# Kernel optimization log

Hardware: AMD Instinct MI355X
Metric: run time of the kernel (lower is better)

## Reference

```python
import jax, jax.numpy as jnp
import numpy as np

SEQ_LEN = 16384
IN_DIM = 2048
STATE_DIM = 2048


def setup_inputs() -> dict:
    key = jax.random.key(0)
    k_xs, k_lam, k_win, k_c, k_d = jax.random.split(key, 5)
    xs = jax.random.normal(k_xs, (SEQ_LEN, IN_DIM), dtype=jnp.float32)
    # diagonal state-transition values in (0, 1) for stability
    lam = jax.random.uniform(k_lam, (STATE_DIM,), dtype=jnp.float32)
    w_in = jax.random.normal(k_win, (STATE_DIM, IN_DIM), dtype=jnp.float32) / np.float32(np.sqrt(IN_DIM))
    c_out = jax.random.normal(k_c, (IN_DIM, STATE_DIM), dtype=jnp.float32) / np.float32(np.sqrt(STATE_DIM))
    d_skip = jax.random.normal(k_d, (IN_DIM,), dtype=jnp.float32)
    return {"xs": xs, "lam": lam, "w_in": w_in, "c_out": c_out, "d_skip": d_skip}


def _ssm_cell(a, b):
    # Faithful replication of BaseSSMLayer.ssm_cell (including its use of
    # matrix_pow_i * matrix_pow_i for the first component, exactly as in source).
    matrix_pow_i, bx_i = a
    matrix_pow_j, bx_j = b
    return (matrix_pow_i * matrix_pow_i, matrix_pow_j * bx_i + bx_j)


def reference(xs, lam, w_in, c_out, d_skip):
    seq_len = xs.shape[0]
    # discretize: broadcast diagonal lambda over the sequence -> [L, N]
    lambda_elements = jnp.broadcast_to(lam, (seq_len, lam.shape[0]))
    # preprocess_inputs: vmap(w_in @ x) == xs @ w_in.T  -> [L, N]
    w_in_xs = jnp.einsum('li,ni->ln', xs, w_in)
    _, hs = jax.lax.associative_scan(_ssm_cell, (lambda_elements, w_in_xs))
    # postprocess: y_t = C h_t + D * x_t  -> [L, in_dim]
    return jnp.einsum('ln,on->lo', hs, c_out) + xs * d_skip
```

## Files before the change

kernel.cpp:

```cpp
#include <hip/hip_runtime.h>
#include <hip/hip_bf16.h>

#define SEQ   16384
#define DIM   2048
#define CHUNK 256
#define NCHUNK (SEQ / CHUNK)

typedef __attribute__((ext_vector_type(8))) short  short8;
typedef __attribute__((ext_vector_type(4))) short  short4v;
typedef __attribute__((ext_vector_type(4))) float  floatx4;

static __device__ __forceinline__ float bf2f(short s) {
    return __uint_as_float(((unsigned)(unsigned short)s) << 16);
}
static __device__ __forceinline__ short f2bf(float f) {
    unsigned u = __float_as_uint(f);
    u += 0x7fff + ((u >> 16) & 1);
    return (short)(u >> 16);
}

__global__ void cast_kernel(const float* __restrict__ in, short* __restrict__ out, int n4) {
    int i = blockIdx.x * blockDim.x + threadIdx.x;
    if (i >= n4) return;
    float4 v = ((const float4*)in)[i];
    short4v s;
    s.x = f2bf(v.x); s.y = f2bf(v.y); s.z = f2bf(v.z); s.w = f2bf(v.w);
    ((short4v*)out)[i] = s;
}

template<int FUSE>
__global__ __launch_bounds__(256, 2)
void gemm_bt(const short* __restrict__ A, const short* __restrict__ B,
             short* __restrict__ Cbf, float* __restrict__ Cf,
             const float* __restrict__ xs, const float* __restrict__ dskip)
{
    constexpr int K = DIM;
    __shared__ alignas(16) short As[128 * 32];
    __shared__ alignas(16) short Bs[128 * 32];

    const int tid = threadIdx.x;
    const int m0  = blockIdx.y * 128;
    const int n0  = blockIdx.x * 128;

    const int c0 = tid, c1 = tid + 256;
    const short* ga0 = A + (size_t)(m0 + (c0 >> 2)) * K + (c0 & 3) * 8;
    const short* ga1 = A + (size_t)(m0 + (c1 >> 2)) * K + (c1 & 3) * 8;
    const short* gb0 = B + (size_t)(n0 + (c0 >> 2)) * K + (c0 & 3) * 8;
    const short* gb1 = B + (size_t)(n0 + (c1 >> 2)) * K + (c1 & 3) * 8;
    short* la0 = &As[c0 * 8];
    short* la1 = &As[c1 * 8];
    short* lb0 = &Bs[c0 * 8];
    short* lb1 = &Bs[c1 * 8];

    const int lane = tid & 63;
    const int wv   = tid >> 6;
    const int wm   = (wv >> 1) * 64;
    const int wn   = (wv & 1) * 64;
    const int l16  = lane & 15;
    const int quad = lane >> 4;

    floatx4 acc[4][4] = {};

    for (int kk = 0; kk < K; kk += 32) {
        __builtin_amdgcn_global_load_lds(ga0 + kk, la0, 16, 0, 0);
        __builtin_amdgcn_global_load_lds(ga1 + kk, la1, 16, 0, 0);
        __builtin_amdgcn_global_load_lds(gb0 + kk, lb0, 16, 0, 0);
        __builtin_amdgcn_global_load_lds(gb1 + kk, lb1, 16, 0, 0);
        __syncthreads();

        short8 aV[4], bV[4];
        #pragma unroll
        for (int i = 0; i < 4; i++)
            aV[i] = *(const short8*)&As[(wm + i * 16 + l16) * 32 + quad * 8];
        #pragma unroll
        for (int i = 0; i < 4; i++)
            bV[i] = *(const short8*)&Bs[(wn + i * 16 + l16) * 32 + quad * 8];

        #pragma unroll
        for (int mi = 0; mi < 4; mi++)
            #pragma unroll
            for (int ni = 0; ni < 4; ni++)
                acc[mi][ni] = __builtin_amdgcn_mfma_f32_16x16x32_bf16(
                    aV[mi], bV[ni], acc[mi][ni], 0, 0, 0);
        __syncthreads();
    }

    if (FUSE == 0) {
        #pragma unroll
        for (int mi = 0; mi < 4; mi++) {
            int rb = m0 + wm + mi * 16 + quad * 4;
            #pragma unroll
            for (int ni = 0; ni < 4; ni++) {
                int cc = n0 + wn + ni * 16 + l16;
                #pragma unroll
                for (int r = 0; r < 4; r++)
                    Cbf[(size_t)(rb + r) * DIM + cc] = f2bf(acc[mi][ni][r]);
            }
        }
    } else {
        float dsk[4];
        #pragma unroll
        for (int ni = 0; ni < 4; ni++) dsk[ni] = dskip[n0 + wn + ni * 16 + l16];
        #pragma unroll
        for (int mi = 0; mi < 4; mi++) {
            int rb = m0 + wm + mi * 16 + quad * 4;
            #pragma unroll
            for (int ni = 0; ni < 4; ni++) {
                int cc = n0 + wn + ni * 16 + l16;
                #pragma unroll
                for (int r = 0; r < 4; r++) {
                    size_t idx = (size_t)(rb + r) * DIM + cc;
                    Cf[idx] = acc[mi][ni][r] + xs[idx] * dsk[ni];
                }
            }
        }
    }
}

__global__ void scan_pass1(const short* __restrict__ bx, const float* __restrict__ lam,
                           float* __restrict__ blockLast)
{
    int n     = blockIdx.x * 256 + threadIdx.x;
    int chunk = blockIdx.y;
    float lm  = lam[n];
    const short* p = bx + (size_t)chunk * CHUNK * DIM + n;
    float h = 0.f;
    #pragma unroll 8
    for (int i = 0; i < CHUNK; i++)
        h = fmaf(lm, h, bf2f(p[(size_t)i * DIM]));
    blockLast[(size_t)chunk * DIM + n] = h;
}

__global__ void scan_pass2(float* __restrict__ blockLast, const float* __restrict__ lam)
{
    int n    = blockIdx.x * 256 + threadIdx.x;
    float lm = lam[n];
    float p  = lm;
    #pragma unroll
    for (int i = 0; i < 8; i++) p = p * p;
    float carry = 0.f;
    for (int c = 0; c < NCHUNK; c++) {
        float t = blockLast[(size_t)c * DIM + n];
        blockLast[(size_t)c * DIM + n] = carry;
        carry = fmaf(p, carry, t);
    }
}

__global__ void scan_pass3(short* __restrict__ bxh, const float* __restrict__ lam,
                           const float* __restrict__ carry)
{
    int n     = blockIdx.x * 256 + threadIdx.x;
    int chunk = blockIdx.y;
    float lm  = lam[n];
    float h   = carry[(size_t)chunk * DIM + n];
    short* p  = bxh + (size_t)chunk * CHUNK * DIM + n;
    #pragma unroll 8
    for (int i = 0; i < CHUNK; i++) {
        h = fmaf(lm, h, bf2f(p[(size_t)i * DIM]));
        p[(size_t)i * DIM] = f2bf(h);
    }
}

extern "C" void kernel_launch(void* const* d_in, const int* in_sizes, int n_in,
                              void* d_out, int out_size, void* d_ws, size_t ws_size,
                              hipStream_t stream)
{
    const float* xs    = (const float*)d_in[0];
    const float* lam   = (const float*)d_in[1];
    const float* w_in  = (const float*)d_in[2];
    const float* c_out = (const float*)d_in[3];
    const float* dskip = (const float*)d_in[4];
    float* out = (float*)d_out;

    char*  ws    = (char*)d_ws;
    short* bxh   = (short*)ws;
    short* w_bf  = (short*)(ws + (size_t)64 * 1024 * 1024);
    short* c_bf  = (short*)(ws + (size_t)72 * 1024 * 1024);
    float* blkl  = (float*)(ws + (size_t)80 * 1024 * 1024);
    short* xs_bf = (short*)d_out;

    cast_kernel<<<SEQ * DIM / 4 / 256, 256, 0, stream>>>(xs, xs_bf, SEQ * DIM / 4);
    cast_kernel<<<DIM * DIM / 4 / 256, 256, 0, stream>>>(w_in, w_bf, DIM * DIM / 4);
    cast_kernel<<<DIM * DIM / 4 / 256, 256, 0, stream>>>(c_out, c_bf, DIM * DIM / 4);

    dim3 ggrid(DIM / 128, SEQ / 128);
    gemm_bt<0><<<ggrid, 256, 0, stream>>>(xs_bf, w_bf, bxh, nullptr, nullptr, nullptr);

    dim3 sgrid(DIM / 256, NCHUNK);
    scan_pass1<<<sgrid, 256, 0, stream>>>(bxh, lam, blkl);
    scan_pass2<<<DIM / 256, 256, 0, stream>>>(blkl, lam);
    scan_pass3<<<sgrid, 256, 0, stream>>>(bxh, lam, blkl);

    gemm_bt<1><<<ggrid, 256, 0, stream>>>(bxh, c_bf, nullptr, out, xs, dskip);
}
```

Baseline: 629.1 us.

## Rewrite GEMM as 256x256 double-buffered swizzled pipeline and vectorize scan

Replaces the 128x128, 256-thread GEMM with a 256x256 tile, 512-thread kernel. It uses BK=64, double-buffered LDS with XOR swizzling, interleaved async global-to-LDS staging, and MFMA phases with raised wave priority and explicit waitcnt/barriers. The scan kernels now process two state channels per thread with 32-bit loads and stores, the chunk size is halved, and the carry buffer moves into unused output memory. This aims to raise MFMA utilization and cut LDS and global load overhead, at the cost of large LDS use (128KB per block), complex fragile synchronisation, and reliance on spare output space.

New measurement: 571.2 us. 9.2% less time.

```diff
diff --git a/kernel.cpp b/kernel.cpp
--- a/kernel.cpp
+++ b/kernel.cpp
@@ -1,9 +1,8 @@
 #include <hip/hip_runtime.h>
-#include <hip/hip_bf16.h>
 
 #define SEQ   16384
 #define DIM   2048
-#define CHUNK 256
+#define CHUNK 128
 #define NCHUNK (SEQ / CHUNK)
 
 typedef __attribute__((ext_vector_type(8))) short  short8;
@@ -28,89 +27,174 @@
     ((short4v*)out)[i] = s;
 }
 
+
+#define BAR   __builtin_amdgcn_s_barrier()
+#define PRIO1 __builtin_amdgcn_s_setprio(1)
+#define PRIO0 __builtin_amdgcn_s_setprio(0)
+#define LGKM0 do { asm volatile("s_waitcnt lgkmcnt(0)" ::: "memory"); \
+                   __builtin_amdgcn_sched_barrier(0); } while (0)
+#define VMC6  asm volatile("s_waitcnt vmcnt(6)" ::: "memory")
+#define VMC0  asm volatile("s_waitcnt vmcnt(0)" ::: "memory")
+
+#define STAGE_A(b, h, t) do { \
+    const short* _s = Abase + (size_t)(h) * 128 * K + (size_t)(t) * 64; \
+    __builtin_amdgcn_global_load_lds(_s + gOff0, &As[b][h][c0 * 8], 16, 0, 0); \
+    __builtin_amdgcn_global_load_lds(_s + gOff1, &As[b][h][c1 * 8], 16, 0, 0); \
+} while (0)
+#define STAGE_B(b, h, t) do { \
+    const short* _s = Bbase + (size_t)(h) * 128 * K + (size_t)(t) * 64; \
+    __builtin_amdgcn_global_load_lds(_s + gOff0, &Bs[b][h][c0 * 8], 16, 0, 0); \
+    __builtin_amdgcn_global_load_lds(_s + gOff1, &Bs[b][h][c1 * 8], 16, 0, 0); \
+} while (0)
+
+#define LDA(b, mh) \
+    _Pragma("unroll") \
+    for (int mi = 0; mi < 4; mi++) { \
+        _Pragma("unroll") \
+        for (int ks = 0; ks < 2; ks++) \
+            aV[mi][ks] = *(const short8*)&As[b][mh][(arow + mi * 16) * 64 + \
+                                                    ((((ks << 2) | quad) ^ sx) << 3)]; \
+    }
+#define LDB(dst, b, nh) \
+    _Pragma("unroll") \
+    for (int ni = 0; ni < 2; ni++) { \
+        _Pragma("unroll") \
+        for (int ks = 0; ks < 2; ks++) \
+            dst[ni][ks] = *(const short8*)&Bs[b][nh][(brow + ni * 16) * 64 + \
+                                                     ((((ks << 2) | quad) ^ sx) << 3)]; \
+    }
+#define MMA(mh, nh, bR) \
+    _Pragma("unroll") \
+    for (int mi = 0; mi < 4; mi++) { \
+        _Pragma("unroll") \
+        for (int ni = 0; ni < 2; ni++) { \
+            acc[mh][nh][mi][ni] = __builtin_amdgcn_mfma_f32_16x16x32_bf16( \
+                aV[mi][0], bR[ni][0], acc[mh][nh][mi][ni], 0, 0, 0); \
+            acc[mh][nh][mi][ni] = __builtin_amdgcn_mfma_f32_16x16x32_bf16( \
+                aV[mi][1], bR[ni][1], acc[mh][nh][mi][ni], 0, 0, 0); \
+        } \
+    }
+
 template<int FUSE>
-__global__ __launch_bounds__(256, 2)
+__global__ __launch_bounds__(512, 2)
 void gemm_bt(const short* __restrict__ A, const short* __restrict__ B,
              short* __restrict__ Cbf, float* __restrict__ Cf,
              const float* __restrict__ xs, const float* __restrict__ dskip)
 {
-    constexpr int K = DIM;
-    __shared__ alignas(16) short As[128 * 32];
-    __shared__ alignas(16) short Bs[128 * 32];
+    constexpr int K  = DIM;
+    constexpr int NT = K / 64;
+
+    __shared__ alignas(16) short As[2][2][128 * 64];
+    __shared__ alignas(16) short Bs[2][2][128 * 64];
 
     const int tid = threadIdx.x;
-    const int m0  = blockIdx.y * 128;
-    const int n0  = blockIdx.x * 128;
-
-    const int c0 = tid, c1 = tid + 256;
-    const short* ga0 = A + (size_t)(m0 + (c0 >> 2)) * K + (c0 & 3) * 8;
-    const short* ga1 = A + (size_t)(m0 + (c1 >> 2)) * K + (c1 & 3) * 8;
-    const short* gb0 = B + (size_t)(n0 + (c0 >> 2)) * K + (c0 & 3) * 8;
-    const short* gb1 = B + (size_t)(n0 + (c1 >> 2)) * K + (c1 & 3) * 8;
-    short* la0 = &As[c0 * 8];
-    short* la1 = &As[c1 * 8];
-    short* lb0 = &Bs[c0 * 8];
-    short* lb1 = &Bs[c1 * 8];
+    const int m0  = blockIdx.y * 256;
+    const int n0  = blockIdx.x * 256;
 
     const int lane = tid & 63;
     const int wv   = tid >> 6;
-    const int wm   = (wv >> 1) * 64;
-    const int wn   = (wv & 1) * 64;
+    const int wrow = wv >> 2;
+    const int wcol = wv & 3;
     const int l16  = lane & 15;
     const int quad = lane >> 4;
-
-    floatx4 acc[4][4] = {};
-
-    for (int kk = 0; kk < K; kk += 32) {
-        __builtin_amdgcn_global_load_lds(ga0 + kk, la0, 16, 0, 0);
-        __builtin_amdgcn_global_load_lds(ga1 + kk, la1, 16, 0, 0);
-        __builtin_amdgcn_global_load_lds(gb0 + kk, lb0, 16, 0, 0);
-        __builtin_amdgcn_global_load_lds(gb1 + kk, lb1, 16, 0, 0);
-        __syncthreads();
-
-        short8 aV[4], bV[4];
-        #pragma unroll
-        for (int i = 0; i < 4; i++)
-            aV[i] = *(const short8*)&As[(wm + i * 16 + l16) * 32 + quad * 8];
-        #pragma unroll
-        for (int i = 0; i < 4; i++)
-            bV[i] = *(const short8*)&Bs[(wn + i * 16 + l16) * 32 + quad * 8];
-
-        #pragma unroll
-        for (int mi = 0; mi < 4; mi++)
-            #pragma unroll
-            for (int ni = 0; ni < 4; ni++)
-                acc[mi][ni] = __builtin_amdgcn_mfma_f32_16x16x32_bf16(
-                    aV[mi], bV[ni], acc[mi][ni], 0, 0, 0);
-        __syncthreads();
-    }
+    const int sx   = l16 & 7;
+    const int arow = wrow * 64 + l16;
+    const int brow = wcol * 32 + l16;
+
+    const int c0 = tid, c1 = tid + 512;
+    const int r0 = c0 >> 3, r1 = c1 >> 3;
+    const size_t gOff0 = (size_t)r0 * K + (size_t)((((c0 & 7) ^ (r0 & 7))) * 8);
+    const size_t gOff1 = (size_t)r1 * K + (size_t)((((c1 & 7) ^ (r1 & 7))) * 8);
+    const short* Abase = A + (size_t)m0 * K;
+    const short* Bbase = B + (size_t)n0 * K;
+
+    short8  aV[4][2], bA[2][2], bB[2][2];
+    floatx4 acc[2][2][4][2] = {};
+
+    STAGE_A(0, 0, 0); STAGE_B(0, 0, 0); STAGE_B(0, 1, 0); STAGE_A(0, 1, 0);
+    STAGE_A(1, 0, 1); STAGE_B(1, 0, 1); STAGE_B(1, 1, 1);
+    VMC6;
+    BAR;
+
+    for (int i = 0; i < NT / 2; ++i) {
+        const int t1 = 2 * i + 1;
+        const int t2 = (2 * i + 2) & (NT - 1);
+        const int t3 = (2 * i + 3) & (NT - 1);
+
+        LDA(0, 0); LDB(bA, 0, 0); STAGE_A(1, 1, t1);
+        BAR; LGKM0;
+        PRIO1; MMA(0, 0, bA); PRIO0;
+        BAR;
+        LDB(bB, 0, 1); STAGE_A(0, 0, t2);
+        BAR; LGKM0;
+        PRIO1; MMA(0, 1, bB); PRIO0;
+        BAR;
+        LDA(0, 1); STAGE_B(0, 0, t2);
+        BAR; LGKM0;
+        PRIO1; MMA(1, 0, bA); PRIO0;
+        BAR;
+        STAGE_B(0, 1, t2);
+        BAR;
+        PRIO1; MMA(1, 1, bB); PRIO0;
+        VMC6;
+        BAR;
+        LDA(1, 0); LDB(bA, 1, 0); STAGE_A(0, 1, t2);
+        BAR; LGKM0;
+        PRIO1; MMA(0, 0, bA); PRIO0;
+        BAR;
+        LDB(bB, 1, 1); STAGE_A(1, 0, t3);
+        BAR; LGKM0;
+        PRIO1; MMA(0, 1, bB); PRIO0;
+        BAR;
+        LDA(1, 1); STAGE_B(1, 0, t3);
+        BAR; LGKM0;
+        PRIO1; MMA(1, 0, bA); PRIO0;
+        BAR;
+        STAGE_B(1, 1, t3);
+        BAR;
+        PRIO1; MMA(1, 1, bB); PRIO0;
+        VMC6;
+        BAR;
+    }
+    VMC0;
 
     if (FUSE == 0) {
         #pragma unroll
+        for (int mh = 0; mh < 2; mh++)
+        #pragma unroll
         for (int mi = 0; mi < 4; mi++) {
-            int rb = m0 + wm + mi * 16 + quad * 4;
-            #pragma unroll
-            for (int ni = 0; ni < 4; ni++) {
-                int cc = n0 + wn + ni * 16 + l16;
+            const int rb = m0 + wrow * 64 + mh * 128 + mi * 16 + quad * 4;
+            #pragma unroll
+            for (int nh = 0; nh < 2; nh++)
+            #pragma unroll
+            for (int ni = 0; ni < 2; ni++) {
+                const int cc = n0 + wcol * 32 + nh * 128 + ni * 16 + l16;
                 #pragma unroll
                 for (int r = 0; r < 4; r++)
-                    Cbf[(size_t)(rb + r) * DIM + cc] = f2bf(acc[mi][ni][r]);
+                    Cbf[(size_t)(rb + r) * DIM + cc] = f2bf(acc[mh][nh][mi][ni][r]);
             }
         }
     } else {
-        float dsk[4];
-        #pragma unroll
-        for (int ni = 0; ni < 4; ni++) dsk[ni] = dskip[n0 + wn + ni * 16 + l16];
+        float dsk[2][2];
+        #pragma unroll
+        for (int nh = 0; nh < 2; nh++)
+        #pragma unroll
+        for (int ni = 0; ni < 2; ni++)
+            dsk[nh][ni] = dskip[n0 + wcol * 32 + nh * 128 + ni * 16 + l16];
+        #pragma unroll
+        for (int mh = 0; mh < 2; mh++)
         #pragma unroll
         for (int mi = 0; mi < 4; mi++) {
-            int rb = m0 + wm + mi * 16 + quad * 4;
-            #pragma unroll
-            for (int ni = 0; ni < 4; ni++) {
-                int cc = n0 + wn + ni * 16 + l16;
+            const int rb = m0 + wrow * 64 + mh * 128 + mi * 16 + quad * 4;
+            #pragma unroll
+            for (int nh = 0; nh < 2; nh++)
+            #pragma unroll
+            for (int ni = 0; ni < 2; ni++) {
+                const int cc = n0 + wcol * 32 + nh * 128 + ni * 16 + l16;
                 #pragma unroll
                 for (int r = 0; r < 4; r++) {
                     size_t idx = (size_t)(rb + r) * DIM + cc;
-                    Cf[idx] = acc[mi][ni][r] + xs[idx] * dsk[ni];
+                    Cf[idx] = acc[mh][nh][mi][ni][r] + xs[idx] * dsk[nh][ni];
                 }
             }
         }
@@ -120,44 +204,58 @@
 __global__ void scan_pass1(const short* __restrict__ bx, const float* __restrict__ lam,
                            float* __restrict__ blockLast)
 {
-    int n     = blockIdx.x * 256 + threadIdx.x;
+    int n2    = blockIdx.x * 256 + threadIdx.x;
+    int n     = n2 * 2;
     int chunk = blockIdx.y;
-    float lm  = lam[n];
-    const short* p = bx + (size_t)chunk * CHUNK * DIM + n;
-    float h = 0.f;
-    #pragma unroll 8
-    for (int i = 0; i < CHUNK; i++)
-        h = fmaf(lm, h, bf2f(p[(size_t)i * DIM]));
-    blockLast[(size_t)chunk * DIM + n] = h;
+    float lm0 = lam[n], lm1 = lam[n + 1];
+    const unsigned* p = (const unsigned*)(bx + (size_t)chunk * CHUNK * DIM) + n2;
+    float h0 = 0.f, h1 = 0.f;
+    #pragma unroll 16
+    for (int i = 0; i < CHUNK; i++) {
+        unsigned v = p[(size_t)i * (DIM / 2)];
+        h0 = fmaf(lm0, h0, bf2f((short)(v & 0xffffu)));
+        h1 = fmaf(lm1, h1, bf2f((short)(v >> 16)));
+    }
+    float2 o; o.x = h0; o.y = h1;
+    *(float2*)&blockLast[(size_t)chunk * DIM + n] = o;
 }
 
 __global__ void scan_pass2(float* __restrict__ blockLast, const float* __restrict__ lam)
 {
-    int n    = blockIdx.x * 256 + threadIdx.x;
-    float lm = lam[n];
-    float p  = lm;
+    int n2 = blockIdx.x * 256 + threadIdx.x;
+    int n  = n2 * 2;
+    float lm0 = lam[n], lm1 = lam[n + 1];
+    float p0 = lm0, p1 = lm1;
     #pragma unroll
-    for (int i = 0; i < 8; i++) p = p * p;
-    float carry = 0.f;
+    for (int i = 0; i < 7; i++) { p0 *= p0; p1 *= p1; }
+    float c0 = 0.f, c1 = 0.f;
     for (int c = 0; c < NCHUNK; c++) {
-        float t = blockLast[(size_t)c * DIM + n];
-        blockLast[(size_t)c * DIM + n] = carry;
-        carry = fmaf(p, carry, t);
+        float2* q = (float2*)&blockLast[(size_t)c * DIM + n];
+        float2 t = *q;
+        float2 w; w.x = c0; w.y = c1;
+        *q = w;
+        c0 = fmaf(p0, c0, t.x);
+        c1 = fmaf(p1, c1, t.y);
     }
 }
 
 __global__ void scan_pass3(short* __restrict__ bxh, const float* __restrict__ lam,
                            const float* __restrict__ carry)
 {
-    int n     = blockIdx.x * 256 + threadIdx.x;
+    int n2    = blockIdx.x * 256 + threadIdx.x;
+    int n     = n2 * 2;
     int chunk = blockIdx.y;
-    float lm  = lam[n];
-    float h   = carry[(size_t)chunk * DIM + n];
-    short* p  = bxh + (size_t)chunk * CHUNK * DIM + n;
-    #pragma unroll 8
+    float lm0 = lam[n], lm1 = lam[n + 1];
+    float h0  = carry[(size_t)chunk * DIM + n];
+    float h1  = carry[(size_t)chunk * DIM + n + 1];
+    unsigned* p = (unsigned*)(bxh + (size_t)chunk * CHUNK * DIM) + n2;
+    #pragma unroll 16
     for (int i = 0; i < CHUNK; i++) {
-        h = fmaf(lm, h, bf2f(p[(size_t)i * DIM]));
-        p[(size_t)i * DIM] = f2bf(h);
+        unsigned v = p[(size_t)i * (DIM / 2)];
+        h0 = fmaf(lm0, h0, bf2f((short)(v & 0xffffu)));
+        h1 = fmaf(lm1, h1, bf2f((short)(v >> 16)));
+        p[(size_t)i * (DIM / 2)] = (unsigned)(unsigned short)f2bf(h0)
+                                 | ((unsigned)(unsigned short)f2bf(h1) << 16);
     }
 }
 
@@ -176,20 +274,20 @@
     short* bxh   = (short*)ws;
     short* w_bf  = (short*)(ws + (size_t)64 * 1024 * 1024);
     short* c_bf  = (short*)(ws + (size_t)72 * 1024 * 1024);
-    float* blkl  = (float*)(ws + (size_t)80 * 1024 * 1024);
     short* xs_bf = (short*)d_out;
+    float* blkl  = (float*)((char*)d_out + (size_t)100 * 1024 * 1024);
 
     cast_kernel<<<SEQ * DIM / 4 / 256, 256, 0, stream>>>(xs, xs_bf, SEQ * DIM / 4);
     cast_kernel<<<DIM * DIM / 4 / 256, 256, 0, stream>>>(w_in, w_bf, DIM * DIM / 4);
     cast_kernel<<<DIM * DIM / 4 / 256, 256, 0, stream>>>(c_out, c_bf, DIM * DIM / 4);
 
-    dim3 ggrid(DIM / 128, SEQ / 128);
-    gemm_bt<0><<<ggrid, 256, 0, stream>>>(xs_bf, w_bf, bxh, nullptr, nullptr, nullptr);
-
-    dim3 sgrid(DIM / 256, NCHUNK);
+    dim3 ggrid(DIM / 256, SEQ / 256);
+    gemm_bt<0><<<ggrid, 512, 0, stream>>>(xs_bf, w_bf, bxh, nullptr, nullptr, nullptr);
+
+    dim3 sgrid(DIM / 512, NCHUNK);
     scan_pass1<<<sgrid, 256, 0, stream>>>(bxh, lam, blkl);
-    scan_pass2<<<DIM / 256, 256, 0, stream>>>(blkl, lam);
+    scan_pass2<<<DIM / 512, 256, 0, stream>>>(blkl, lam);
     scan_pass3<<<sgrid, 256, 0, stream>>>(bxh, lam, blkl);
 
-    gemm_bt<1><<<ggrid, 256, 0, stream>>>(bxh, c_bf, nullptr, out, xs, dskip);
-}
+    gemm_bt<1><<<ggrid, 512, 0, stream>>>(bxh, c_bf, nullptr, out, xs, dskip);
+}
```
